# Optimization experiments

Hardware: AMD Instinct MI355X
Metric: run time of the kernel (lower is better)

The kernel has to match this reference:

```python
import jax, jax.numpy as jnp
import numpy as np

N = 20000   # num_nodes
D = 128     # node_dim
H = 128     # hidden_dim (also per-head channels, PyG out_channels is per-head)
EV = 64     # event_dim
NH = 4      # heads
E = 250000  # num edges
NT = 8      # num_event_types
K = 4       # active event types


def setup_inputs() -> dict:
    key = jax.random.key(0)
    ks = jax.random.split(key, 24)
    def w(i, shape, s=0.05):
        return jax.random.normal(ks[i], shape, dtype=jnp.float32) * s
    z = lambda shape: jnp.zeros(shape, jnp.float32)
    o = lambda shape: jnp.ones(shape, jnp.float32)
    return {
        "node_ids": jnp.arange(N, dtype=jnp.int32),
        "event_type_ids": jax.random.randint(ks[0], (K,), 0, NT, dtype=jnp.int32),
        "src": jax.random.randint(ks[1], (E,), 0, N, dtype=jnp.int32),
        "dst": jax.random.randint(ks[2], (E,), 0, N, dtype=jnp.int32),
        "event_features": jax.random.normal(ks[3], (EV,), dtype=jnp.float32),
        "event_intensity": jax.random.uniform(ks[4], (K,), dtype=jnp.float32),
        "node_emb_table": w(5, (N, D), 1.0),
        "event_type_table": w(6, (NT, H), 0.5),
        "ev_w1": w(7, (EV, H)), "ev_b1": z((H,)), "ev_g1": o((H,)), "ev_bt1": z((H,)),
        "ev_w2": w(8, (H, H)), "ev_b2": z((H,)), "ev_g2": o((H,)), "ev_bt2": z((H,)),
        "wq": w(9, (D + H, NH * H)), "bq": z((NH * H,)),
        "wk": w(10, (D + H, NH * H)), "bk": z((NH * H,)),
        "wv": w(11, (D + H, NH * H)), "bv": z((NH * H,)),
        "wskip": w(12, (D + H, H)), "bskip": z((H,)),
        "g0_w": w(13, (H, NH * H)), "g0_as": w(14, (NH, H), 0.1), "g0_ad": w(15, (NH, H), 0.1), "g0_b": z((H,)),
        "g1_w": w(16, (H, NH * H)), "g1_as": w(17, (NH, H), 0.1), "g1_ad": w(18, (NH, H), 0.1), "g1_b": z((H,)),
        "wih": w(19, (H, 4 * H)), "whh": w(20, (H, 4 * H)), "bih": z((4 * H,)), "bhh": z((4 * H,)),
    }


def layer_norm(x, g, b, eps=1e-5):
    mu = jnp.mean(x, axis=-1, keepdims=True)
    var = jnp.mean(jnp.square(x - mu), axis=-1, keepdims=True)
    return (x - mu) * jax.lax.rsqrt(var + eps) * g + b


def segment_softmax(logits, seg, n):
    # logits: [E, NH]; softmax over edges sharing the same destination seg id
    m = jax.ops.segment_max(logits, seg, num_segments=n)
    m = jnp.where(jnp.isfinite(m), m, 0.0)  # guard empty segments
    e = jnp.exp(logits - m[seg])
    s = jax.ops.segment_sum(e, seg, num_segments=n)
    return e / (s[seg] + 1e-16)


def _forward(node_ids, event_type_ids, src, dst,
             event_features, event_intensity, node_emb_table, event_type_table,
             ev_w1, ev_b1, ev_g1, ev_bt1, ev_w2, ev_b2, ev_g2, ev_bt2,
             wq, bq, wk, bk, wv, bv, wskip, bskip,
             g0_w, g0_as, g0_ad, g0_b, g1_w, g1_as, g1_ad, g1_b,
             wih, whh, bih, bhh):
    node_emb = node_emb_table[node_ids]                                      # [N, D]
    # event encoder MLP (dropout off / eval mode)
    e = jax.nn.relu(layer_norm(event_features @ ev_w1 + ev_b1, ev_g1, ev_bt1))
    e = jax.nn.relu(layer_norm(e @ ev_w2 + ev_b2, ev_g2, ev_bt2))            # [H]
    # intensity-weighted mean of active event-type embeddings
    e = e + jnp.mean(event_type_table[event_type_ids] * event_intensity[:, None], axis=0)
    x = jnp.concatenate([node_emb, jnp.broadcast_to(e, (N, H))], axis=1)     # [N, D+H]

    # --- TransformerConv (heads=NH, concat=False -> head mean, root_weight skip) ---
    q = (x @ wq + bq).reshape(N, NH, H)
    k = (x @ wk + bk).reshape(N, NH, H)
    v = (x @ wv + bv).reshape(N, NH, H)
    alpha = jnp.sum(q[dst] * k[src], axis=-1) / jnp.sqrt(jnp.float32(H))     # [E, NH]
    alpha = segment_softmax(alpha, dst, N)
    agg = jax.ops.segment_sum(v[src] * alpha[..., None], dst, num_segments=N)  # [N, NH, H]
    x = agg.mean(axis=1) + x @ wskip + bskip                                 # [N, H]

    sl = jnp.arange(N, dtype=src.dtype)
    src2 = jnp.concatenate([src, sl])
    dst2 = jnp.concatenate([dst, sl])
    for w_, asrc, adst, b_ in ((g0_w, g0_as, g0_ad, g0_b), (g1_w, g1_as, g1_ad, g1_b)):
        xh = (x @ w_).reshape(N, NH, H)
        a_s = jnp.sum(xh * asrc, axis=-1)                                    # [N, NH]
        a_d = jnp.sum(xh * adst, axis=-1)
        ee = jax.nn.leaky_relu(a_s[src2] + a_d[dst2], 0.2)                   # [E+N, NH]
        a = segment_softmax(ee, dst2, N)
        out = jax.ops.segment_sum(xh[src2] * a[..., None], dst2, num_segments=N)
        x = jax.nn.relu(out.mean(axis=1) + b_)                               # [N, H]

    # --- batched LSTMCell, zero initial (h, c); torch gate order i, f, g, o ---
    h0 = jnp.zeros((N, H), x.dtype)
    c0 = jnp.zeros((N, H), x.dtype)
    gates = x @ wih + bih + h0 @ whh + bhh                                   # [N, 4H]
    gi, gf, gg, go = jnp.split(gates, 4, axis=-1)
    c = jax.nn.sigmoid(gf) * c0 + jax.nn.sigmoid(gi) * jnp.tanh(gg)
    h = jax.nn.sigmoid(go) * jnp.tanh(c)
    return h, c


def reference(node_ids, event_type_ids, src, dst,
              event_features, event_intensity, node_emb_table, event_type_table,
              ev_w1, ev_b1, ev_g1, ev_bt1, ev_w2, ev_b2, ev_g2, ev_bt2,
              wq, bq, wk, bk, wv, bv, wskip, bskip,
              g0_w, g0_as, g0_ad, g0_b, g1_w, g1_as, g1_ad, g1_b,
              wih, whh, bih, bhh):
    return _forward(node_ids, event_type_ids, src, dst,
                    event_features, event_intensity, node_emb_table, event_type_table,
                    ev_w1, ev_b1, ev_g1, ev_bt1, ev_w2, ev_b2, ev_g2, ev_bt2,
                    wq, bq, wk, bk, wv, bv, wskip, bskip,
                    g0_w, g0_as, g0_ad, g0_b, g1_w, g1_as, g1_ad, g1_b,
                    wih, whh, bih, bhh)
```

## Files before the change

kernel.cpp:

```cpp
#include <hip/hip_runtime.h>
#include <math.h>

#define D_DIM 128
#define H_DIM 128
#define QKV_N 1664
#define SQRT_H_INV 0.08838834764831845f

typedef unsigned short u16;
typedef unsigned short ushort8v __attribute__((ext_vector_type(8)));
typedef __bf16 bf16x8 __attribute__((ext_vector_type(8)));
typedef float f32x4 __attribute__((ext_vector_type(4)));

__device__ __forceinline__ float grp16_sum(float v) {
  v += __shfl_xor(v, 1);
  v += __shfl_xor(v, 2);
  v += __shfl_xor(v, 4);
  v += __shfl_xor(v, 8);
  return v;
}

__device__ __forceinline__ void split_bf16(float x, u16& h, u16& l) {
  __bf16 hb = (__bf16)x;
  float rm = x - (float)hb;
  __bf16 lb = (__bf16)rm;
  h = __builtin_bit_cast(u16, hb);
  l = __builtin_bit_cast(u16, lb);
}

__global__ __launch_bounds__(128) void k_event(
    const float* __restrict__ ef, int EV,
    const float* __restrict__ w1, const float* __restrict__ b1,
    const float* __restrict__ g1, const float* __restrict__ bt1,
    const float* __restrict__ w2, const float* __restrict__ b2,
    const float* __restrict__ g2, const float* __restrict__ bt2,
    const float* __restrict__ ett, const int* __restrict__ etid,
    const float* __restrict__ inten, int K,
    float* __restrict__ e_out)
{
  __shared__ float sh[H_DIM];
  __shared__ float red[H_DIM];
  const int t = threadIdx.x;

  float acc = b1[t];
  for (int i = 0; i < EV; ++i) acc += ef[i] * w1[i * H_DIM + t];

  red[t] = acc; __syncthreads();
  for (int s = 64; s > 0; s >>= 1) { if (t < s) red[t] += red[t + s]; __syncthreads(); }
  float mu = red[0] / H_DIM; __syncthreads();
  float d = acc - mu;
  red[t] = d * d; __syncthreads();
  for (int s = 64; s > 0; s >>= 1) { if (t < s) red[t] += red[t + s]; __syncthreads(); }
  float var = red[0] / H_DIM; __syncthreads();
  float y = d * rsqrtf(var + 1e-5f) * g1[t] + bt1[t];
  y = fmaxf(y, 0.f);
  sh[t] = y; __syncthreads();

  float acc2 = b2[t];
  for (int i = 0; i < H_DIM; ++i) acc2 += sh[i] * w2[i * H_DIM + t];

  red[t] = acc2; __syncthreads();
  for (int s = 64; s > 0; s >>= 1) { if (t < s) red[t] += red[t + s]; __syncthreads(); }
  mu = red[0] / H_DIM; __syncthreads();
  d = acc2 - mu;
  red[t] = d * d; __syncthreads();
  for (int s = 64; s > 0; s >>= 1) { if (t < s) red[t] += red[t + s]; __syncthreads(); }
  var = red[0] / H_DIM; __syncthreads();
  float y2 = d * rsqrtf(var + 1e-5f) * g2[t] + bt2[t];
  y2 = fmaxf(y2, 0.f);

  float m = 0.f;
  for (int k = 0; k < K; ++k) m += ett[etid[k] * H_DIM + t] * inten[k];
  e_out[t] = y2 + m / (float)K;
}

__global__ __launch_bounds__(256) void k_cvec(
    const float* __restrict__ e,
    const float* __restrict__ wq, const float* __restrict__ bq,
    const float* __restrict__ wk, const float* __restrict__ bk,
    const float* __restrict__ wv, const float* __restrict__ bv,
    const float* __restrict__ wskip, const float* __restrict__ bskip,
    float* __restrict__ cvec)
{
  __shared__ float es[H_DIM];
  const int t = threadIdx.x;
  if (t < H_DIM) es[t] = e[t];
  __syncthreads();
  int j = blockIdx.x * 256 + t;
  if (j >= QKV_N) return;
  const float* W; const float* b; int col; int stride;
  if (j < 512)       { W = wq;    b = bq;    col = j;        stride = 512; }
  else if (j < 1024) { W = wk;    b = bk;    col = j - 512;  stride = 512; }
  else if (j < 1536) { W = wv;    b = bv;    col = j - 1024; stride = 512; }
  else               { W = wskip; b = bskip; col = j - 1536; stride = 128; }
  float a = b[col];
  for (int i = 0; i < H_DIM; ++i) a += es[i] * W[(D_DIM + i) * stride + col];
  cvec[j] = a;
}

__global__ __launch_bounds__(256) void k_pack(
    const float* __restrict__ wq, const float* __restrict__ wk,
    const float* __restrict__ wv, const float* __restrict__ wskip,
    float* __restrict__ B1)
{
  int idx = blockIdx.x * 256 + threadIdx.x;
  if (idx >= D_DIM * QKV_N) return;
  int i = idx / QKV_N, j = idx - i * QKV_N;
  float v;
  if (j < 512)       v = wq[i * 512 + j];
  else if (j < 1024) v = wk[i * 512 + (j - 512)];
  else if (j < 1536) v = wv[i * 512 + (j - 1024)];
  else               v = wskip[i * 128 + (j - 1536)];
  B1[idx] = v;
}

__global__ __launch_bounds__(256) void k_cvec2(
    const float* __restrict__ bih, const float* __restrict__ bhh,
    float* __restrict__ cvec2)
{
  int j = blockIdx.x * 256 + threadIdx.x;
  if (j < 512) cvec2[j] = bih[j] + bhh[j];
}

__global__ __launch_bounds__(256) void k_split_a(
    const float* __restrict__ A, const int* __restrict__ ids,
    u16* __restrict__ hi, u16* __restrict__ lo, int M, int Mpad)
{
  int idx = blockIdx.x * 256 + threadIdx.x;
  if (idx >= Mpad * 16) return;
  int row = idx >> 4, g = idx & 15;
  int gp = g ^ (row & 7);
  size_t dst = (size_t)row * 128 + gp * 8;
  if (row < M) {
    int ar = ids ? ids[row] : row;
    const float* srcp = A + (size_t)ar * 128 + g * 8;
#pragma unroll
    for (int j = 0; j < 8; ++j) {
      u16 h, l;
      split_bf16(srcp[j], h, l);
      hi[dst + j] = h; lo[dst + j] = l;
    }
  } else {
#pragma unroll
    for (int j = 0; j < 8; ++j) { hi[dst + j] = 0; lo[dst + j] = 0; }
  }
}

__global__ __launch_bounds__(256) void k_split_bt(
    const float* __restrict__ W,
    u16* __restrict__ hi, u16* __restrict__ lo, int Nc)
{
  int idx = blockIdx.x * 256 + threadIdx.x;
  if (idx >= Nc * 16) return;
  int n = idx >> 4, g = idx & 15;
  int gp = g ^ (n & 7);
  size_t dst = (size_t)n * 128 + gp * 8;
#pragma unroll
  for (int j = 0; j < 8; ++j) {
    u16 h, l;
    split_bf16(W[(size_t)(g * 8 + j) * Nc + n], h, l);
    hi[dst + j] = h; lo[dst + j] = l;
  }
}

__global__ __launch_bounds__(256, 2) void mfma_gemm(
    const u16* __restrict__ Ahi, const u16* __restrict__ Alo,
    const u16* __restrict__ Bhi, const u16* __restrict__ Blo,
    const float* __restrict__ cvec, float* __restrict__ C, int M, int Nn,
    u16* __restrict__ bf_out, int bf_lo, int bf_hi, int bf_stride, int skipf32)
{
  __shared__ u16 lds[32768];
  u16* As_hi = lds;
  u16* As_lo = lds + 8192;
  u16* Bs_hi = lds + 16384;
  u16* Bs_lo = lds + 24576;

  const int t = threadIdx.x;
  const int bm = blockIdx.y * 128;
  const int bn = blockIdx.x * 128;
  const int lane = t & 63;
  const int wid = t >> 6;
  const int wr = wid >> 1, wc = wid & 1;
  const int abase = wr * 64 + (lane & 15);
  const int bbase = wc * 64 + (lane & 15);

  int srow[4], sg[4];
#pragma unroll
  for (int i = 0; i < 4; ++i) {
    int idx = i * 256 + t;
    srow[i] = idx >> 3;
    sg[i] = idx & 7;
  }

  ushort8v ra_h[4], ra_l[4], rb_h[4], rb_l[4];

#pragma unroll
  for (int i = 0; i < 4; ++i) {
    size_t ga = (size_t)(bm + srow[i]) * 128 + sg[i] * 8;
    size_t gb = (size_t)(bn + srow[i]) * 128 + sg[i] * 8;
    ra_h[i] = *(const ushort8v*)&Ahi[ga];
    ra_l[i] = *(const ushort8v*)&Alo[ga];
    rb_h[i] = *(const ushort8v*)&Bhi[gb];
    rb_l[i] = *(const ushort8v*)&Blo[gb];
  }
#pragma unroll
  for (int i = 0; i < 4; ++i) {
    int lo_ = srow[i] * 64 + sg[i] * 8;
    *(ushort8v*)&As_hi[lo_] = ra_h[i];
    *(ushort8v*)&As_lo[lo_] = ra_l[i];
    *(ushort8v*)&Bs_hi[lo_] = rb_h[i];
    *(ushort8v*)&Bs_lo[lo_] = rb_l[i];
  }
  __syncthreads();

#pragma unroll
  for (int i = 0; i < 4; ++i) {
    size_t ga = (size_t)(bm + srow[i]) * 128 + 64 + sg[i] * 8;
    size_t gb = (size_t)(bn + srow[i]) * 128 + 64 + sg[i] * 8;
    ra_h[i] = *(const ushort8v*)&Ahi[ga];
    ra_l[i] = *(const ushort8v*)&Alo[ga];
    rb_h[i] = *(const ushort8v*)&Bhi[gb];
    rb_l[i] = *(const ushort8v*)&Blo[gb];
  }

  f32x4 acc[4][4];
  const f32x4 zero = {0.f, 0.f, 0.f, 0.f};
#pragma unroll
  for (int i = 0; i < 4; ++i)
#pragma unroll
    for (int j = 0; j < 4; ++j) acc[i][j] = zero;

#pragma unroll
  for (int ks = 0; ks < 2; ++ks) {
    const int gl = (((ks & 1) << 2) + (lane >> 4)) ^ (lane & 7);
    bf16x8 ah[4], al[4], bh[4], bl[4];
#pragma unroll
    for (int i = 0; i < 4; ++i) {
      int ra = (abase + i * 16) * 64 + gl * 8;
      ah[i] = *(const bf16x8*)&As_hi[ra];
      al[i] = *(const bf16x8*)&As_lo[ra];
      int rb = (bbase + i * 16) * 64 + gl * 8;
      bh[i] = *(const bf16x8*)&Bs_hi[rb];
      bl[i] = *(const bf16x8*)&Bs_lo[rb];
    }
#pragma unroll
    for (int i = 0; i < 4; ++i)
#pragma unroll
      for (int j = 0; j < 4; ++j) {
        acc[i][j] = __builtin_amdgcn_mfma_f32_16x16x32_bf16(ah[i], bh[j], acc[i][j], 0, 0, 0);
        acc[i][j] = __builtin_amdgcn_mfma_f32_16x16x32_bf16(ah[i], bl[j], acc[i][j], 0, 0, 0);
        acc[i][j] = __builtin_amdgcn_mfma_f32_16x16x32_bf16(al[i], bh[j], acc[i][j], 0, 0, 0);
      }
  }
  __syncthreads();

#pragma unroll
  for (int i = 0; i < 4; ++i) {
    int lo_ = srow[i] * 64 + sg[i] * 8;
    *(ushort8v*)&As_hi[lo_] = ra_h[i];
    *(ushort8v*)&As_lo[lo_] = ra_l[i];
    *(ushort8v*)&Bs_hi[lo_] = rb_h[i];
    *(ushort8v*)&Bs_lo[lo_] = rb_l[i];
  }
  __syncthreads();

#pragma unroll
  for (int ks = 2; ks < 4; ++ks) {
    const int gl = (((ks & 1) << 2) + (lane >> 4)) ^ (lane & 7);
    bf16x8 ah[4], al[4], bh[4], bl[4];
#pragma unroll
    for (int i = 0; i < 4; ++i) {
      int ra = (abase + i * 16) * 64 + gl * 8;
      ah[i] = *(const bf16x8*)&As_hi[ra];
      al[i] = *(const bf16x8*)&As_lo[ra];
      int rb = (bbase + i * 16) * 64 + gl * 8;
      bh[i] = *(const bf16x8*)&Bs_hi[rb];
      bl[i] = *(const bf16x8*)&Bs_lo[rb];
    }
#pragma unroll
    for (int i = 0; i < 4; ++i)
#pragma unroll
      for (int j = 0; j < 4; ++j) {
        acc[i][j] = __builtin_amdgcn_mfma_f32_16x16x32_bf16(ah[i], bh[j], acc[i][j], 0, 0, 0);
        acc[i][j] = __builtin_amdgcn_mfma_f32_16x16x32_bf16(ah[i], bl[j], acc[i][j], 0, 0, 0);
        acc[i][j] = __builtin_amdgcn_mfma_f32_16x16x32_bf16(al[i], bh[j], acc[i][j], 0, 0, 0);
      }
  }

  const int rq = (lane >> 4) << 2;
  const int cq = lane & 15;
#pragma unroll
  for (int j = 0; j < 4; ++j) {
    int col = bn + wc * 64 + j * 16 + cq;
    float cv = cvec ? cvec[col] : 0.f;
    bool inbf = bf_out && col >= bf_lo && col < bf_hi;
    bool wf32 = !(inbf && skipf32);
#pragma unroll
    for (int i = 0; i < 4; ++i) {
#pragma unroll
      for (int r = 0; r < 4; ++r) {
        int row = bm + wr * 64 + i * 16 + rq + r;
        if (row < M) {
          float val = acc[i][j][r] + cv;
          if (wf32) C[(size_t)row * Nn + col] = val;
          if (inbf) bf_out[(size_t)row * bf_stride + (col - bf_lo)] =
              __builtin_bit_cast(u16, (__bf16)val);
        }
      }
    }
  }
}

__global__ __launch_bounds__(256) void k_zero(int* __restrict__ p, int n) {
  int i = blockIdx.x * 256 + threadIdx.x;
  if (i < n) p[i] = 0;
}
__global__ __launch_bounds__(256) void k_count(
    const int* __restrict__ dst, int* __restrict__ counts, int E) {
  int e = blockIdx.x * 256 + threadIdx.x;
  if (e < E) atomicAdd(&counts[dst[e]], 1);
}
__global__ __launch_bounds__(1024) void k_scan(
    const int* __restrict__ counts, int* __restrict__ offs,
    int* __restrict__ cursor, int N)
{
  __shared__ int wsum[16];
  const int t = threadIdx.x;
  const int lane = t & 63;
  const int wid = t >> 6;
  int running = 0;
  for (int base = 0; base < N; base += 1024) {
    int v = (base + t < N) ? counts[base + t] : 0;
    int incl = v;
#pragma unroll
    for (int s = 1; s < 64; s <<= 1) {
      int u = __shfl_up(incl, s);
      if (lane >= s) incl += u;
    }
    if (lane == 63) wsum[wid] = incl;
    __syncthreads();
    if (wid == 0) {
      int w = (lane < 16) ? wsum[lane] : 0;
#pragma unroll
      for (int s = 1; s < 16; s <<= 1) {
        int u = __shfl_up(w, s);
        if (lane >= s) w += u;
      }
      if (lane < 16) wsum[lane] = w;
    }
    __syncthreads();
    int wpre = (wid > 0) ? wsum[wid - 1] : 0;
    int tot = wsum[15];
    int inclg = incl + wpre;
    if (base + t < N) {
      offs[base + t + 1] = running + inclg;
      cursor[base + t] = running + inclg - v;
    }
    running += tot;
    __syncthreads();
  }
  if (t == 0) offs[0] = 0;
}
__global__ __launch_bounds__(256) void k_fill(
    const int* __restrict__ src, const int* __restrict__ dst,
    int* __restrict__ cursor, int* __restrict__ csr_src, int E) {
  int e = blockIdx.x * 256 + threadIdx.x;
  if (e < E) {
    int slot = atomicAdd(&cursor[dst[e]], 1);
    csr_src[slot] = src[e];
  }
}

__global__ __launch_bounds__(256) void k_tconv(
    const float* __restrict__ C1, const u16* __restrict__ KV,
    const int* __restrict__ offs, const int* __restrict__ csr_src,
    u16* __restrict__ Xhi, u16* __restrict__ Xlo, int N)
{
  const int wid = threadIdx.x >> 6;
  const int lane = threadIdx.x & 63;
  const int node = blockIdx.x * 4 + wid;
  if (node >= N) {
    if (lane < 16) {
      size_t dst = (size_t)node * 128 + (size_t)((lane ^ (node & 7)) * 8);
#pragma unroll
      for (int j = 0; j < 8; ++j) { Xhi[dst + j] = 0; Xlo[dst + j] = 0; }
    }
    return;
  }
  const float* crow = C1 + (size_t)node * QKV_N;
  float q[8];
  {
    float4 q0 = *(const float4*)(crow + lane * 8);
    float4 q1 = *(const float4*)(crow + lane * 8 + 4);
    q[0]=q0.x; q[1]=q0.y; q[2]=q0.z; q[3]=q0.w;
    q[4]=q1.x; q[5]=q1.y; q[6]=q1.z; q[7]=q1.w;
  }
  const int beg = offs[node], end = offs[node + 1];
  float mx = -1e30f;
  float ssum = 0.f;
  float acc[8] = {0.f,0.f,0.f,0.f,0.f,0.f,0.f,0.f};

  int e = beg;
  for (; e + 4 <= end; e += 4) {
    int s0 = csr_src[e];
    int s1 = csr_src[e + 1];
    int s2 = csr_src[e + 2];
    int s3 = csr_src[e + 3];
    const u16* r0 = KV + (size_t)s0 * 1024 + lane * 8;
    const u16* r1 = KV + (size_t)s1 * 1024 + lane * 8;
    const u16* r2 = KV + (size_t)s2 * 1024 + lane * 8;
    const u16* r3 = KV + (size_t)s3 * 1024 + lane * 8;
    bf16x8 k0 = *(const bf16x8*)(r0);
    bf16x8 k1 = *(const bf16x8*)(r1);
    bf16x8 k2 = *(const bf16x8*)(r2);
    bf16x8 k3 = *(const bf16x8*)(r3);
    bf16x8 v0 = *(const bf16x8*)(r0 + 512);
    bf16x8 v1 = *(const bf16x8*)(r1 + 512);
    bf16x8 v2 = *(const bf16x8*)(r2 + 512);
    bf16x8 v3 = *(const bf16x8*)(r3 + 512);
    float p0 = 0.f, p1 = 0.f, p2 = 0.f, p3 = 0.f;
#pragma unroll
    for (int j = 0; j < 8; ++j) {
      p0 += q[j] * (float)k0[j];
      p1 += q[j] * (float)k1[j];
      p2 += q[j] * (float)k2[j];
      p3 += q[j] * (float)k3[j];
    }
    p0 = grp16_sum(p0) * SQRT_H_INV;
    p1 = grp16_sum(p1) * SQRT_H_INV;
    p2 = grp16_sum(p2) * SQRT_H_INV;
    p3 = grp16_sum(p3) * SQRT_H_INV;
    float nm = fmaxf(fmaxf(fmaxf(p0, p1), fmaxf(p2, p3)), mx);
    float sc = expf(mx - nm);
    float w0 = expf(p0 - nm);
    float w1 = expf(p1 - nm);
    float w2 = expf(p2 - nm);
    float w3 = expf(p3 - nm);
    ssum = ssum * sc + (w0 + w1) + (w2 + w3);
#pragma unroll
    for (int j = 0; j < 8; ++j)
      acc[j] = acc[j] * sc + (w0 * (float)v0[j] + w1 * (float)v1[j])
                           + (w2 * (float)v2[j] + w3 * (float)v3[j]);
    mx = nm;
  }
  for (; e < end; ++e) {
    int s0 = csr_src[e];
    const u16* r0 = KV + (size_t)s0 * 1024 + lane * 8;
    bf16x8 ka = *(const bf16x8*)(r0);
    bf16x8 va = *(const bf16x8*)(r0 + 512);
    float p0 = 0.f;
#pragma unroll
    for (int j = 0; j < 8; ++j) p0 += q[j] * (float)ka[j];
    p0 = grp16_sum(p0) * SQRT_H_INV;
    float nm = fmaxf(mx, p0);
    float sc = expf(mx - nm);
    float w0 = expf(p0 - nm);
    ssum = ssum * sc + w0;
#pragma unroll
    for (int j = 0; j < 8; ++j)
      acc[j] = acc[j] * sc + w0 * (float)va[j];
    mx = nm;
  }

  float inv = 1.f / (ssum + 1e-16f);
#pragma unroll
  for (int j = 0; j < 8; ++j) acc[j] *= inv;
#pragma unroll
  for (int j = 0; j < 8; ++j) {
    acc[j] += __shfl_xor(acc[j], 16);
    acc[j] += __shfl_xor(acc[j], 32);
  }
  if (lane < 16) {
    const float* sk = crow + 1536 + lane * 8;
    size_t dst = (size_t)node * 128 + (size_t)((lane ^ (node & 7)) * 8);
#pragma unroll
    for (int j = 0; j < 8; ++j) {
      float x = 0.25f * acc[j] + sk[j];
      u16 h, l;
      split_bf16(x, h, l);
      Xhi[dst + j] = h; Xlo[dst + j] = l;
    }
  }
}

__global__ __launch_bounds__(256) void k_gat_ad(
    const float* __restrict__ xh, const float* __restrict__ as_w,
    const float* __restrict__ ad_w, float* __restrict__ a_s,
    float* __restrict__ a_d, int N)
{
  const int wid = threadIdx.x >> 6;
  const int lane = threadIdx.x & 63;
  const int node = blockIdx.x * 4 + wid;
  if (node >= N) return;
  const int head = lane >> 4;
  const int c0 = (lane & 15) * 8;
  const float* xr = xh + (size_t)node * 512 + lane * 8;
  float4 x0 = *(const float4*)(xr);
  float4 x1_ = *(const float4*)(xr + 4);
  const float* aw = as_w + head * 128 + c0;
  const float* dw = ad_w + head * 128 + c0;
  float s1 = x0.x*aw[0] + x0.y*aw[1] + x0.z*aw[2] + x0.w*aw[3]
           + x1_.x*aw[4] + x1_.y*aw[5] + x1_.z*aw[6] + x1_.w*aw[7];
  float s2 = x0.x*dw[0] + x0.y*dw[1] + x0.z*dw[2] + x0.w*dw[3]
           + x1_.x*dw[4] + x1_.y*dw[5] + x1_.z*dw[6] + x1_.w*dw[7];
  s1 = grp16_sum(s1);
  s2 = grp16_sum(s2);
  if ((lane & 15) == 0) {
    a_s[node * 4 + head] = s1;
    a_d[node * 4 + head] = s2;
  }
}

__global__ __launch_bounds__(256) void k_gat_agg(
    const float* __restrict__ xh, const u16* __restrict__ xhb,
    const float* __restrict__ a_s, const float* __restrict__ a_d,
    const int* __restrict__ offs, const int* __restrict__ csr_src,
    const float* __restrict__ bias,
    u16* __restrict__ Xhi, u16* __restrict__ Xlo, int N)
{
  const int wid = threadIdx.x >> 6;
  const int lane = threadIdx.x & 63;
  const int node = blockIdx.x * 4 + wid;
  if (node >= N) {
    if (lane < 16) {
      size_t dst = (size_t)node * 128 + (size_t)((lane ^ (node & 7)) * 8);
#pragma unroll
      for (int j = 0; j < 8; ++j) { Xhi[dst + j] = 0; Xlo[dst + j] = 0; }
    }
    return;
  }
  const int head = lane >> 4;
  const float adn = a_d[node * 4 + head];
  const float asn = a_s[node * 4 + head];
  float lself = asn + adn;
  lself = lself >= 0.f ? lself : 0.2f * lself;

  float mx = lself;
  float ssum = 1.f;
  float acc[8];
  {
    const float* xr = xh + (size_t)node * 512 + lane * 8;
    float4 x0 = *(const float4*)(xr);
    float4 x1_ = *(const float4*)(xr + 4);
    acc[0]=x0.x; acc[1]=x0.y; acc[2]=x0.z; acc[3]=x0.w;
    acc[4]=x1_.x; acc[5]=x1_.y; acc[6]=x1_.z; acc[7]=x1_.w;
  }

  const int beg = offs[node], end = offs[node + 1];
  int e = beg;
  for (; e + 4 <= end; e += 4) {
    int s0 = csr_src[e];
    int s1 = csr_src[e + 1];
    int s2 = csr_src[e + 2];
    int s3 = csr_src[e + 3];
    float l0 = a_s[s0 * 4 + head];
    float l1 = a_s[s1 * 4 + head];
    float l2 = a_s[s2 * 4 + head];
    float l3 = a_s[s3 * 4 + head];
    const u16* r0 = xhb + (size_t)s0 * 512 + lane * 8;
    const u16* r1 = xhb + (size_t)s1 * 512 + lane * 8;
    const u16* r2 = xhb + (size_t)s2 * 512 + lane * 8;
    const u16* r3 = xhb + (size_t)s3 * 512 + lane * 8;
    bf16x8 xa = *(const bf16x8*)(r0);
    bf16x8 xb = *(const bf16x8*)(r1);
    bf16x8 xc = *(const bf16x8*)(r2);
    bf16x8 xd = *(const bf16x8*)(r3);
    l0 += adn; l1 += adn; l2 += adn; l3 += adn;
    l0 = l0 >= 0.f ? l0 : 0.2f * l0;
    l1 = l1 >= 0.f ? l1 : 0.2f * l1;
    l2 = l2 >= 0.f ? l2 : 0.2f * l2;
    l3 = l3 >= 0.f ? l3 : 0.2f * l3;
    float nm = fmaxf(fmaxf(fmaxf(l0, l1), fmaxf(l2, l3)), mx);
    float sc = expf(mx - nm);
    float w0 = expf(l0 - nm);
    float w1 = expf(l1 - nm);
    float w2 = expf(l2 - nm);
    float w3 = expf(l3 - nm);
    ssum = ssum * sc + (w0 + w1) + (w2 + w3);
#pragma unroll
    for (int j = 0; j < 8; ++j)
      acc[j] = acc[j] * sc + (w0 * (float)xa[j] + w1 * (float)xb[j])
                           + (w2 * (float)xc[j] + w3 * (float)xd[j]);
    mx = nm;
  }
  for (; e < end; ++e) {
    int s0 = csr_src[e];
    float l0 = a_s[s0 * 4 + head] + adn;
    l0 = l0 >= 0.f ? l0 : 0.2f * l0;
    const u16* r0 = xhb + (size_t)s0 * 512 + lane * 8;
    bf16x8 xa = *(const bf16x8*)(r0);
    float nm = fmaxf(mx, l0);
    float sc = expf(mx - nm);
    float w0 = expf(l0 - nm);
    ssum = ssum * sc + w0;
#pragma unroll
    for (int j = 0; j < 8; ++j)
      acc[j] = acc[j] * sc + w0 * (float)xa[j];
    mx = nm;
  }

  float inv = 1.f / (ssum + 1e-16f);
#pragma unroll
  for (int j = 0; j < 8; ++j) acc[j] *= inv;
#pragma unroll
  for (int j = 0; j < 8; ++j) {
    acc[j] += __shfl_xor(acc[j], 16);
    acc[j] += __shfl_xor(acc[j], 32);
  }
  if (lane < 16) {
    const float* b = bias + lane * 8;
    size_t dst = (size_t)node * 128 + (size_t)((lane ^ (node & 7)) * 8);
#pragma unroll
    for (int j = 0; j < 8; ++j) {
      float x = fmaxf(0.25f * acc[j] + b[j], 0.f);
      u16 h, l;
      split_bf16(x, h, l);
      Xhi[dst + j] = h; Xlo[dst + j] = l;
    }
  }
}

__global__ __launch_bounds__(256) void k_lstm(
    const float* __restrict__ gates, float* __restrict__ out, int N)
{
  int idx = blockIdx.x * 256 + threadIdx.x;
  if (idx >= N * 128) return;
  int n = idx >> 7, c = idx & 127;
  const float* g = gates + (size_t)n * 512;
  float gi = g[c], gg = g[256 + c], go = g[384 + c];
  float cv = (1.f / (1.f + expf(-gi))) * tanhf(gg);
  float hv = (1.f / (1.f + expf(-go))) * tanhf(cv);
  out[idx] = hv;
  out[(size_t)N * 128 + idx] = cv;
}

extern "C" void kernel_launch(void* const* d_in, const int* in_sizes, int n_in,
                              void* d_out, int out_size, void* d_ws, size_t ws_size,
                              hipStream_t stream) {
  const int*   node_ids = (const int*)d_in[0];
  const int*   etid     = (const int*)d_in[1];
  const int*   src      = (const int*)d_in[2];
  const int*   dst      = (const int*)d_in[3];
  const float* ef       = (const float*)d_in[4];
  const float* inten    = (const float*)d_in[5];
  const float* nemb     = (const float*)d_in[6];
  const float* ett      = (const float*)d_in[7];
  const float* ev_w1 = (const float*)d_in[8],  *ev_b1 = (const float*)d_in[9];
  const float* ev_g1 = (const float*)d_in[10], *ev_bt1 = (const float*)d_in[11];
  const float* ev_w2 = (const float*)d_in[12], *ev_b2 = (const float*)d_in[13];
  const float* ev_g2 = (const float*)d_in[14], *ev_bt2 = (const float*)d_in[15];
  const float* wq = (const float*)d_in[16], *bq = (const float*)d_in[17];
  const float* wk = (const float*)d_in[18], *bk = (const float*)d_in[19];
  const float* wv = (const float*)d_in[20], *bv = (const float*)d_in[21];
  const float* wskip = (const float*)d_in[22], *bskip = (const float*)d_in[23];
  const float* g0_w = (const float*)d_in[24], *g0_as = (const float*)d_in[25];
  const float* g0_ad = (const float*)d_in[26], *g0_b = (const float*)d_in[27];
  const float* g1_w = (const float*)d_in[28], *g1_as = (const float*)d_in[29];
  const float* g1_ad = (const float*)d_in[30], *g1_b = (const float*)d_in[31];
  const float* wih = (const float*)d_in[32];
  const float* bih = (const float*)d_in[34], *bhh = (const float*)d_in[35];

  const int N = in_sizes[0];
  const int K = in_sizes[1];
  const int E = in_sizes[2];
  const int EV = in_sizes[4];

  const int gridMy = (N + 127) / 128;
  const int Npad = gridMy * 128;

  float* ws = (float*)d_ws;
  size_t o = 0;
  float* e_vec = ws + o; o += 128;
  float* cvec1 = ws + o; o += QKV_N;
  float* cvec2 = ws + o; o += 512;
  float* B1    = ws + o; o += (size_t)128 * QKV_N;
  float* C1    = ws + o; o += (size_t)N * QKV_N;
  float* xh    = ws + o; o += (size_t)N * 512;
  u16* Ahi  = (u16*)(ws + o); o += (size_t)Npad * 64;
  u16* Alo  = (u16*)(ws + o); o += (size_t)Npad * 64;
  u16* XShi = (u16*)(ws + o); o += (size_t)Npad * 64;
  u16* XSlo = (u16*)(ws + o); o += (size_t)Npad * 64;
  u16* Bqhi = (u16*)(ws + o); o += (size_t)QKV_N * 64;
  u16* Bqlo = (u16*)(ws + o); o += (size_t)QKV_N * 64;
  u16* Bg0hi = (u16*)(ws + o); o += 512 * 64;
  u16* Bg0lo = (u16*)(ws + o); o += 512 * 64;
  u16* Bg1hi = (u16*)(ws + o); o += 512 * 64;
  u16* Bg1lo = (u16*)(ws + o); o += 512 * 64;
  u16* Bwhi  = (u16*)(ws + o); o += 512 * 64;
  u16* Bwlo  = (u16*)(ws + o); o += 512 * 64;
  u16* KV   = (u16*)(ws + o); o += (size_t)Npad * 512;
  u16* xhb  = (u16*)(ws + o); o += (size_t)Npad * 256;
  float* a_s   = ws + o; o += (size_t)N * 4;
  float* a_d   = ws + o; o += (size_t)N * 4;
  int* counts  = (int*)(ws + o); o += N;
  int* offs    = (int*)(ws + o); o += (size_t)N + 1;
  int* cursor  = (int*)(ws + o); o += N;
  int* csr_src = (int*)(ws + o); o += E;

  float* out = (float*)d_out;

  const int nodeBlocks = (N + 3) / 4;
  const int nodeBlocksPad = Npad / 4;

  k_event<<<1, 128, 0, stream>>>(ef, EV, ev_w1, ev_b1, ev_g1, ev_bt1,
                                 ev_w2, ev_b2, ev_g2, ev_bt2,
                                 ett, etid, inten, K, e_vec);
  k_cvec<<<(QKV_N + 255) / 256, 256, 0, stream>>>(e_vec, wq, bq, wk, bk, wv, bv,
                                                  wskip, bskip, cvec1);
  k_pack<<<(D_DIM * QKV_N + 255) / 256, 256, 0, stream>>>(wq, wk, wv, wskip, B1);
  k_cvec2<<<2, 256, 0, stream>>>(bih, bhh, cvec2);

  k_split_a<<<(Npad * 16 + 255) / 256, 256, 0, stream>>>(nemb, node_ids, Ahi, Alo, N, Npad);
  k_split_bt<<<(QKV_N * 16 + 255) / 256, 256, 0, stream>>>(B1, Bqhi, Bqlo, QKV_N);
  k_split_bt<<<(512 * 16 + 255) / 256, 256, 0, stream>>>(g0_w, Bg0hi, Bg0lo, 512);
  k_split_bt<<<(512 * 16 + 255) / 256, 256, 0, stream>>>(g1_w, Bg1hi, Bg1lo, 512);
  k_split_bt<<<(512 * 16 + 255) / 256, 256, 0, stream>>>(wih, Bwhi, Bwlo, 512);

  k_zero<<<(N + 255) / 256, 256, 0, stream>>>(counts, N);
  k_count<<<(E + 255) / 256, 256, 0, stream>>>(dst, counts, E);
  k_scan<<<1, 1024, 0, stream>>>(counts, offs, cursor, N);
  k_fill<<<(E + 255) / 256, 256, 0, stream>>>(src, dst, cursor, csr_src, E);

  mfma_gemm<<<dim3(QKV_N / 128, gridMy), 256, 0, stream>>>(
      Ahi, Alo, Bqhi, Bqlo, cvec1, C1, N, QKV_N,
      KV, 512, 1536, 1024, 1);

  k_tconv<<<nodeBlocksPad, 256, 0, stream>>>(C1, KV, offs, csr_src, XShi, XSlo, N);

  mfma_gemm<<<dim3(4, gridMy), 256, 0, stream>>>(
      XShi, XSlo, Bg0hi, Bg0lo, nullptr, xh, N, 512,
      xhb, 0, 512, 512, 0);
  k_gat_ad<<<nodeBlocks, 256, 0, stream>>>(xh, g0_as, g0_ad, a_s, a_d, N);
  k_gat_agg<<<nodeBlocksPad, 256, 0, stream>>>(xh, xhb, a_s, a_d, offs, csr_src,
                                               g0_b, XShi, XSlo, N);

  mfma_gemm<<<dim3(4, gridMy), 256, 0, stream>>>(
      XShi, XSlo, Bg1hi, Bg1lo, nullptr, xh, N, 512,
      xhb, 0, 512, 512, 0);
  k_gat_ad<<<nodeBlocks, 256, 0, stream>>>(xh, g1_as, g1_ad, a_s, a_d, N);
  k_gat_agg<<<nodeBlocksPad, 256, 0, stream>>>(xh, xhb, a_s, a_d, offs, csr_src,
                                               g1_b, XShi, XSlo, N);

  mfma_gemm<<<dim3(4, gridMy), 256, 0, stream>>>(
      XShi, XSlo, Bwhi, Bwlo, cvec2, xh, N, 512,
      nullptr, 0, 0, 0, 0);
  k_lstm<<<((N * 128) + 255) / 256, 256, 0, stream>>>(xh, out, N);
}
```

Measured before the change: 445.8 us.

## Fuse GAT attention scores into GEMM epilogue, drop f32 outputs and dead LSTM gate

Merges the weight packing, splitting and bias kernels into one k_split_all and one k_cvec_all launch. The QKV GEMM now writes Q/K/V only as bf16 plus a small f32 skip buffer, instead of a full f32 C1 matrix. The GAT GEMMs compute the per-head source and destination attention dot products in the epilogue using LDS atomics, which removes k_gat_ad and the f32 xh writes; gat_agg reads its self term from bf16. The LSTM GEMM skips the forget-gate columns, which are unused because the initial cell state is zero. Together these cut launches and global memory traffic, at the cost of bf16 rounding on Q and the self-feature terms and extra LDS atomics in the epilogue.

```diff
diff --git a/kernel.cpp b/kernel.cpp
--- a/kernel.cpp
+++ b/kernel.cpp
@@ -3,8 +3,12 @@
 
 #define D_DIM 128
 #define H_DIM 128
-#define QKV_N 1664
 #define SQRT_H_INV 0.08838834764831845f
+#define BCOL_QKV 0
+#define BCOL_G0 1664
+#define BCOL_G1 2176
+#define BCOL_W  2688
+#define BCOL_TOT 3072
 
 typedef unsigned short u16;
 typedef unsigned short ushort8v __attribute__((ext_vector_type(8)));
@@ -73,52 +77,62 @@
   e_out[t] = y2 + m / (float)K;
 }
 
-__global__ __launch_bounds__(256) void k_cvec(
+__global__ __launch_bounds__(256) void k_cvec_all(
     const float* __restrict__ e,
     const float* __restrict__ wq, const float* __restrict__ bq,
     const float* __restrict__ wk, const float* __restrict__ bk,
     const float* __restrict__ wv, const float* __restrict__ bv,
     const float* __restrict__ wskip, const float* __restrict__ bskip,
-    float* __restrict__ cvec)
+    const float* __restrict__ bih, const float* __restrict__ bhh,
+    float* __restrict__ cvec1, float* __restrict__ cvec2)
 {
   __shared__ float es[H_DIM];
   const int t = threadIdx.x;
   if (t < H_DIM) es[t] = e[t];
   __syncthreads();
   int j = blockIdx.x * 256 + t;
-  if (j >= QKV_N) return;
-  const float* W; const float* b; int col; int stride;
-  if (j < 512)       { W = wq;    b = bq;    col = j;        stride = 512; }
-  else if (j < 1024) { W = wk;    b = bk;    col = j - 512;  stride = 512; }
-  else if (j < 1536) { W = wv;    b = bv;    col = j - 1024; stride = 512; }
-  else               { W = wskip; b = bskip; col = j - 1536; stride = 128; }
-  float a = b[col];
-  for (int i = 0; i < H_DIM; ++i) a += es[i] * W[(D_DIM + i) * stride + col];
-  cvec[j] = a;
-}
-
-__global__ __launch_bounds__(256) void k_pack(
+  if (j < 1664) {
+    const float* W; const float* b; int col; int stride;
+    if (j < 512)       { W = wq;    b = bq;    col = j;        stride = 512; }
+    else if (j < 1024) { W = wk;    b = bk;    col = j - 512;  stride = 512; }
+    else if (j < 1536) { W = wv;    b = bv;    col = j - 1024; stride = 512; }
+    else               { W = wskip; b = bskip; col = j - 1536; stride = 128; }
+    float a = b[col];
+    for (int i = 0; i < H_DIM; ++i) a += es[i] * W[(D_DIM + i) * stride + col];
+    cvec1[j] = a;
+  } else if (j < 1664 + 384) {
+    int j2 = j - 1664;
+    int src = (j2 < 128) ? j2 : j2 + 128;
+    cvec2[j2] = bih[src] + bhh[src];
+  }
+}
+
+__global__ __launch_bounds__(256) void k_split_all(
     const float* __restrict__ wq, const float* __restrict__ wk,
     const float* __restrict__ wv, const float* __restrict__ wskip,
-    float* __restrict__ B1)
+    const float* __restrict__ g0w, const float* __restrict__ g1w,
+    const float* __restrict__ wih,
+    u16* __restrict__ hi, u16* __restrict__ lo)
 {
   int idx = blockIdx.x * 256 + threadIdx.x;
-  if (idx >= D_DIM * QKV_N) return;
-  int i = idx / QKV_N, j = idx - i * QKV_N;
-  float v;
-  if (j < 512)       v = wq[i * 512 + j];
-  else if (j < 1024) v = wk[i * 512 + (j - 512)];
-  else if (j < 1536) v = wv[i * 512 + (j - 1024)];
-  else               v = wskip[i * 128 + (j - 1536)];
-  B1[idx] = v;
-}
-
-__global__ __launch_bounds__(256) void k_cvec2(
-    const float* __restrict__ bih, const float* __restrict__ bhh,
-    float* __restrict__ cvec2)
-{
-  int j = blockIdx.x * 256 + threadIdx.x;
-  if (j < 512) cvec2[j] = bih[j] + bhh[j];
+  if (idx >= BCOL_TOT * 16) return;
+  int n = idx >> 4, g = idx & 15;
+  const float* W; int col, stride;
+  if (n < 512)        { W = wq;    col = n;        stride = 512; }
+  else if (n < 1024)  { W = wk;    col = n - 512;  stride = 512; }
+  else if (n < 1536)  { W = wv;    col = n - 1024; stride = 512; }
+  else if (n < 1664)  { W = wskip; col = n - 1536; stride = 128; }
+  else if (n < 2176)  { W = g0w;   col = n - 1664; stride = 512; }
+  else if (n < 2688)  { W = g1w;   col = n - 2176; stride = 512; }
+  else { int c = n - 2688; W = wih; col = (c < 128) ? c : c + 128; stride = 512; }
+  int gp = g ^ (n & 7);
+  size_t dst = (size_t)n * 128 + gp * 8;
+#pragma unroll
+  for (int j = 0; j < 8; ++j) {
+    u16 h, l;
+    split_bf16(W[(size_t)(g * 8 + j) * stride + col], h, l);
+    hi[dst + j] = h; lo[dst + j] = l;
+  }
 }
 
 __global__ __launch_bounds__(256) void k_split_a(
@@ -145,28 +159,15 @@
   }
 }
 
-__global__ __launch_bounds__(256) void k_split_bt(
-    const float* __restrict__ W,
-    u16* __restrict__ hi, u16* __restrict__ lo, int Nc)
-{
-  int idx = blockIdx.x * 256 + threadIdx.x;
-  if (idx >= Nc * 16) return;
-  int n = idx >> 4, g = idx & 15;
-  int gp = g ^ (n & 7);
-  size_t dst = (size_t)n * 128 + gp * 8;
-#pragma unroll
-  for (int j = 0; j < 8; ++j) {
-    u16 h, l;
-    split_bf16(W[(size_t)(g * 8 + j) * Nc + n], h, l);
-    hi[dst + j] = h; lo[dst + j] = l;
-  }
-}
-
 __global__ __launch_bounds__(256, 2) void mfma_gemm(
     const u16* __restrict__ Ahi, const u16* __restrict__ Alo,
     const u16* __restrict__ Bhi, const u16* __restrict__ Blo,
-    const float* __restrict__ cvec, float* __restrict__ C, int M, int Nn,
-    u16* __restrict__ bf_out, int bf_lo, int bf_hi, int bf_stride, int skipf32)
+    const float* __restrict__ cvec,
+    u16* __restrict__ bf_out, int bf_cols,
+    float* __restrict__ f32_out, int f32_lo, int ld_f32,
+    const float* __restrict__ asw, const float* __restrict__ adw,
+    float* __restrict__ a_s, float* __restrict__ a_d,
+    int M)
 {
   __shared__ u16 lds[32768];
   u16* As_hi = lds;
@@ -288,23 +289,59 @@
 
   const int rq = (lane >> 4) << 2;
   const int cq = lane & 15;
-#pragma unroll
-  for (int j = 0; j < 4; ++j) {
-    int col = bn + wc * 64 + j * 16 + cq;
-    float cv = cvec ? cvec[col] : 0.f;
-    bool inbf = bf_out && col >= bf_lo && col < bf_hi;
-    bool wf32 = !(inbf && skipf32);
-#pragma unroll
-    for (int i = 0; i < 4; ++i) {
-#pragma unroll
-      for (int r = 0; r < 4; ++r) {
-        int row = bm + wr * 64 + i * 16 + rq + r;
-        if (row < M) {
-          float val = acc[i][j][r] + cv;
-          if (wf32) C[(size_t)row * Nn + col] = val;
-          if (inbf) bf_out[(size_t)row * bf_stride + (col - bf_lo)] =
-              __builtin_bit_cast(u16, (__bf16)val);
+  const int head = bn >> 7;
+
+  float ws_[4], wd_[4];
+  float* redS = (float*)lds;
+  float* redD = ((float*)lds) + 128;
+  if (asw) {
+#pragma unroll
+    for (int j = 0; j < 4; ++j) {
+      int cc = (wc * 64 + j * 16 + cq) & 127;
+      ws_[j] = asw[head * 128 + cc];
+      wd_[j] = adw[head * 128 + cc];
+    }
+    __syncthreads();
+    if (t < 128) { redS[t] = 0.f; }
+    else if (t < 256) { redD[t - 128] = 0.f; }
+    __syncthreads();
+  }
+
+#pragma unroll
+  for (int i = 0; i < 4; ++i) {
+#pragma unroll
+    for (int r = 0; r < 4; ++r) {
+      int rowl = wr * 64 + i * 16 + rq + r;
+      int row = bm + rowl;
+      bool rok = row < M;
+      float ps = 0.f, pd = 0.f;
+#pragma unroll
+      for (int j = 0; j < 4; ++j) {
+        int col = bn + wc * 64 + j * 16 + cq;
+        float a = acc[i][j][r];
+        if (rok) {
+          float val = a + (cvec ? cvec[col] : 0.f);
+          if (bf_out && col < bf_cols)
+            bf_out[(size_t)row * bf_cols + col] =
+                __builtin_bit_cast(u16, (__bf16)val);
+          if (f32_out && col >= f32_lo)
+            f32_out[(size_t)row * ld_f32 + (col - f32_lo)] = val;
         }
+        if (asw) { ps += a * ws_[j]; pd += a * wd_[j]; }
+      }
+      if (asw && rok) {
+        atomicAdd(&redS[rowl], ps);
+        atomicAdd(&redD[rowl], pd);
+      }
+    }
+  }
+  if (asw) {
+    __syncthreads();
+    if (t < 128) {
+      int row = bm + t;
+      if (row < M) {
+        a_s[row * 4 + head] = redS[t];
+        a_d[row * 4 + head] = redD[t];
       }
     }
   }
@@ -371,7 +408,7 @@
 }
 
 __global__ __launch_bounds__(256) void k_tconv(
-    const float* __restrict__ C1, const u16* __restrict__ KV,
+    const u16* __restrict__ QKVp, const float* __restrict__ skipbuf,
     const int* __restrict__ offs, const int* __restrict__ csr_src,
     u16* __restrict__ Xhi, u16* __restrict__ Xlo, int N)
 {
@@ -386,13 +423,11 @@
     }
     return;
   }
-  const float* crow = C1 + (size_t)node * QKV_N;
   float q[8];
   {
-    float4 q0 = *(const float4*)(crow + lane * 8);
-    float4 q1 = *(const float4*)(crow + lane * 8 + 4);
-    q[0]=q0.x; q[1]=q0.y; q[2]=q0.z; q[3]=q0.w;
-    q[4]=q1.x; q[5]=q1.y; q[6]=q1.z; q[7]=q1.w;
+    bf16x8 qv = *(const bf16x8*)(QKVp + (size_t)node * 1536 + lane * 8);
+#pragma unroll
+    for (int j = 0; j < 8; ++j) q[j] = (float)qv[j];
   }
   const int beg = offs[node], end = offs[node + 1];
   float mx = -1e30f;
@@ -405,10 +440,10 @@
     int s1 = csr_src[e + 1];
     int s2 = csr_src[e + 2];
     int s3 = csr_src[e + 3];
-    const u16* r0 = KV + (size_t)s0 * 1024 + lane * 8;
-    const u16* r1 = KV + (size_t)s1 * 1024 + lane * 8;
-    const u16* r2 = KV + (size_t)s2 * 1024 + lane * 8;
-    const u16* r3 = KV + (size_t)s3 * 1024 + lane * 8;
+    const u16* r0 = QKVp + (size_t)s0 * 1536 + 512 + lane * 8;
+    const u16* r1 = QKVp + (size_t)s1 * 1536 + 512 + lane * 8;
+    const u16* r2 = QKVp + (size_t)s2 * 1536 + 512 + lane * 8;
+    const u16* r3 = QKVp + (size_t)s3 * 1536 + 512 + lane * 8;
     bf16x8 k0 = *(const bf16x8*)(r0);
     bf16x8 k1 = *(const bf16x8*)(r1);
     bf16x8 k2 = *(const bf16x8*)(r2);
@@ -444,7 +479,7 @@
   }
   for (; e < end; ++e) {
     int s0 = csr_src[e];
-    const u16* r0 = KV + (size_t)s0 * 1024 + lane * 8;
+    const u16* r0 = QKVp + (size_t)s0 * 1536 + 512 + lane * 8;
     bf16x8 ka = *(const bf16x8*)(r0);
     bf16x8 va = *(const bf16x8*)(r0 + 512);
     float p0 = 0.f;
@@ -470,7 +505,7 @@
     acc[j] += __shfl_xor(acc[j], 32);
   }
   if (lane < 16) {
-    const float* sk = crow + 1536 + lane * 8;
+    const float* sk = skipbuf + (size_t)node * 128 + lane * 8;
     size_t dst = (size_t)node * 128 + (size_t)((lane ^ (node & 7)) * 8);
 #pragma unroll
     for (int j = 0; j < 8; ++j) {
@@ -482,36 +517,8 @@
   }
 }
 
-__global__ __launch_bounds__(256) void k_gat_ad(
-    const float* __restrict__ xh, const float* __restrict__ as_w,
-    const float* __restrict__ ad_w, float* __restrict__ a_s,
-    float* __restrict__ a_d, int N)
-{
-  const int wid = threadIdx.x >> 6;
-  const int lane = threadIdx.x & 63;
-  const int node = blockIdx.x * 4 + wid;
-  if (node >= N) return;
-  const int head = lane >> 4;
-  const int c0 = (lane & 15) * 8;
-  const float* xr = xh + (size_t)node * 512 + lane * 8;
-  float4 x0 = *(const float4*)(xr);
-  float4 x1_ = *(const float4*)(xr + 4);
-  const float* aw = as_w + head * 128 + c0;
-  const float* dw = ad_w + head * 128 + c0;
-  float s1 = x0.x*aw[0] + x0.y*aw[1] + x0.z*aw[2] + x0.w*aw[3]
-           + x1_.x*aw[4] + x1_.y*aw[5] + x1_.z*aw[6] + x1_.w*aw[7];
-  float s2 = x0.x*dw[0] + x0.y*dw[1] + x0.z*dw[2] + x0.w*dw[3]
-           + x1_.x*dw[4] + x1_.y*dw[5] + x1_.z*dw[6] + x1_.w*dw[7];
-  s1 = grp16_sum(s1);
-  s2 = grp16_sum(s2);
-  if ((lane & 15) == 0) {
-    a_s[node * 4 + head] = s1;
-    a_d[node * 4 + head] = s2;
-  }
-}
-
 __global__ __launch_bounds__(256) void k_gat_agg(
-    const float* __restrict__ xh, const u16* __restrict__ xhb,
+    const u16* __restrict__ xhb,
     const float* __restrict__ a_s, const float* __restrict__ a_d,
     const int* __restrict__ offs, const int* __restrict__ csr_src,
     const float* __restrict__ bias,
@@ -538,11 +545,9 @@
   float ssum = 1.f;
   float acc[8];
   {
-    const float* xr = xh + (size_t)node * 512 + lane * 8;
-    float4 x0 = *(const float4*)(xr);
-    float4 x1_ = *(const float4*)(xr + 4);
-    acc[0]=x0.x; acc[1]=x0.y; acc[2]=x0.z; acc[3]=x0.w;
-    acc[4]=x1_.x; acc[5]=x1_.y; acc[6]=x1_.z; acc[7]=x1_.w;
+    bf16x8 xs = *(const bf16x8*)(xhb + (size_t)node * 512 + lane * 8);
+#pragma unroll
+    for (int j = 0; j < 8; ++j) acc[j] = (float)xs[j];
   }
 
   const int beg = offs[node], end = offs[node + 1];
@@ -625,8 +630,8 @@
   int idx = blockIdx.x * 256 + threadIdx.x;
   if (idx >= N * 128) return;
   int n = idx >> 7, c = idx & 127;
-  const float* g = gates + (size_t)n * 512;
-  float gi = g[c], gg = g[256 + c], go = g[384 + c];
+  const float* g = gates + (size_t)n * 384;
+  float gi = g[c], gg = g[128 + c], go = g[256 + c];
   float cv = (1.f / (1.f + expf(-gi))) * tanhf(gg);
   float hv = (1.f / (1.f + expf(-go))) * tanhf(cv);
   out[idx] = hv;
@@ -670,25 +675,18 @@
   float* ws = (float*)d_ws;
   size_t o = 0;
   float* e_vec = ws + o; o += 128;
-  float* cvec1 = ws + o; o += QKV_N;
-  float* cvec2 = ws + o; o += 512;
-  float* B1    = ws + o; o += (size_t)128 * QKV_N;
-  float* C1    = ws + o; o += (size_t)N * QKV_N;
-  float* xh    = ws + o; o += (size_t)N * 512;
+  float* cvec1 = ws + o; o += 1664;
+  float* cvec2 = ws + o; o += 384;
+  u16* Ballhi = (u16*)(ws + o); o += (size_t)BCOL_TOT * 64;
+  u16* Balllo = (u16*)(ws + o); o += (size_t)BCOL_TOT * 64;
   u16* Ahi  = (u16*)(ws + o); o += (size_t)Npad * 64;
   u16* Alo  = (u16*)(ws + o); o += (size_t)Npad * 64;
   u16* XShi = (u16*)(ws + o); o += (size_t)Npad * 64;
   u16* XSlo = (u16*)(ws + o); o += (size_t)Npad * 64;
-  u16* Bqhi = (u16*)(ws + o); o += (size_t)QKV_N * 64;
-  u16* Bqlo = (u16*)(ws + o); o += (size_t)QKV_N * 64;
-  u16* Bg0hi = (u16*)(ws + o); o += 512 * 64;
-  u16* Bg0lo = (u16*)(ws + o); o += 512 * 64;
-  u16* Bg1hi = (u16*)(ws + o); o += 512 * 64;
-  u16* Bg1lo = (u16*)(ws + o); o += 512 * 64;
-  u16* Bwhi  = (u16*)(ws + o); o += 512 * 64;
-  u16* Bwlo  = (u16*)(ws + o); o += 512 * 64;
-  u16* KV   = (u16*)(ws + o); o += (size_t)Npad * 512;
+  u16* QKVp = (u16*)(ws + o); o += (size_t)Npad * 768;
+  float* skipbuf = ws + o; o += (size_t)Npad * 128;
   u16* xhb  = (u16*)(ws + o); o += (size_t)Npad * 256;
+  float* gates = ws + o; o += (size_t)Npad * 384;
   float* a_s   = ws + o; o += (size_t)N * 4;
   float* a_d   = ws + o; o += (size_t)N * 4;
   int* counts  = (int*)(ws + o); o += N;
@@ -697,51 +695,47 @@
   int* csr_src = (int*)(ws + o); o += E;
 
   float* out = (float*)d_out;
-
-  const int nodeBlocks = (N + 3) / 4;
   const int nodeBlocksPad = Npad / 4;
 
   k_event<<<1, 128, 0, stream>>>(ef, EV, ev_w1, ev_b1, ev_g1, ev_bt1,
                                  ev_w2, ev_b2, ev_g2, ev_bt2,
                                  ett, etid, inten, K, e_vec);
-  k_cvec<<<(QKV_N + 255) / 256, 256, 0, stream>>>(e_vec, wq, bq, wk, bk, wv, bv,
-                                                  wskip, bskip, cvec1);
-  k_pack<<<(D_DIM * QKV_N + 255) / 256, 256, 0, stream>>>(wq, wk, wv, wskip, B1);
-  k_cvec2<<<2, 256, 0, stream>>>(bih, bhh, cvec2);
-
+  k_cvec_all<<<8, 256, 0, stream>>>(e_vec, wq, bq, wk, bk, wv, bv,
+                                    wskip, bskip, bih, bhh, cvec1, cvec2);
+  k_split_all<<<(BCOL_TOT * 16) / 256, 256, 0, stream>>>(
+      wq, wk, wv, wskip, g0_w, g1_w, wih, Ballhi, Balllo);
   k_split_a<<<(Npad * 16 + 255) / 256, 256, 0, stream>>>(nemb, node_ids, Ahi, Alo, N, Npad);
-  k_split_bt<<<(QKV_N * 16 + 255) / 256, 256, 0, stream>>>(B1, Bqhi, Bqlo, QKV_N);
-  k_split_bt<<<(512 * 16 + 255) / 256, 256, 0, stream>>>(g0_w, Bg0hi, Bg0lo, 512);
-  k_split_bt<<<(512 * 16 + 255) / 256, 256, 0, stream>>>(g1_w, Bg1hi, Bg1lo, 512);
-  k_split_bt<<<(512 * 16 + 255) / 256, 256, 0, stream>>>(wih, Bwhi, Bwlo, 512);
 
   k_zero<<<(N + 255) / 256, 256, 0, stream>>>(counts, N);
   k_count<<<(E + 255) / 256, 256, 0, stream>>>(dst, counts, E);
   k_scan<<<1, 1024, 0, stream>>>(counts, offs, cursor, N);
   k_fill<<<(E + 255) / 256, 256, 0, stream>>>(src, dst, cursor, csr_src, E);
 
-  mfma_gemm<<<dim3(QKV_N / 128, gridMy), 256, 0, stream>>>(
-      Ahi, Alo, Bqhi, Bqlo, cvec1, C1, N, QKV_N,
-      KV, 512, 1536, 1024, 1);
-
-  k_tconv<<<nodeBlocksPad, 256, 0, stream>>>(C1, KV, offs, csr_src, XShi, XSlo, N);
+  mfma_gemm<<<dim3(13, gridMy), 256, 0, stream>>>(
+      Ahi, Alo, Ballhi + (size_t)BCOL_QKV * 128, Balllo + (size_t)BCOL_QKV * 128,
+      cvec1, QKVp, 1536, skipbuf, 1536, 128,
+      nullptr, nullptr, nullptr, nullptr, N);
+
+  k_tconv<<<nodeBlocksPad, 256, 0, stream>>>(QKVp, skipbuf, offs, csr_src,
+                                             XShi, XSlo, N);
 
   mfma_gemm<<<dim3(4, gridMy), 256, 0, stream>>>(
-      XShi, XSlo, Bg0hi, Bg0lo, nullptr, xh, N, 512,
-      xhb, 0, 512, 512, 0);
-  k_gat_ad<<<nodeBlocks, 256, 0, stream>>>(xh, g0_as, g0_ad, a_s, a_d, N);
-  k_gat_agg<<<nodeBlocksPad, 256, 0, stream>>>(xh, xhb, a_s, a_d, offs, csr_src,
+      XShi, XSlo, Ballhi + (size_t)BCOL_G0 * 128, Balllo + (size_t)BCOL_G0 * 128,
+      nullptr, xhb, 512, nullptr, 0, 0,
+      g0_as, g0_ad, a_s, a_d, N);
+  k_gat_agg<<<nodeBlocksPad, 256, 0, stream>>>(xhb, a_s, a_d, offs, csr_src,
                                                g0_b, XShi, XSlo, N);
 
   mfma_gemm<<<dim3(4, gridMy), 256, 0, stream>>>(
-      XShi, XSlo, Bg1hi, Bg1lo, nullptr, xh, N, 512,
-      xhb, 0, 512, 512, 0);
-  k_gat_ad<<<nodeBlocks, 256, 0, stream>>>(xh, g1_as, g1_ad, a_s, a_d, N);
-  k_gat_agg<<<nodeBlocksPad, 256, 0, stream>>>(xh, xhb, a_s, a_d, offs, csr_src,
+      XShi, XSlo, Ballhi + (size_t)BCOL_G1 * 128, Balllo + (size_t)BCOL_G1 * 128,
+      nullptr, xhb, 512, nullptr, 0, 0,
+      g1_as, g1_ad, a_s, a_d, N);
+  k_gat_agg<<<nodeBlocksPad, 256, 0, stream>>>(xhb, a_s, a_d, offs, csr_src,
                                                g1_b, XShi, XSlo, N);
 
-  mfma_gemm<<<dim3(4, gridMy), 256, 0, stream>>>(
-      XShi, XSlo, Bwhi, Bwlo, cvec2, xh, N, 512,
-      nullptr, 0, 0, 0, 0);
-  k_lstm<<<((N * 128) + 255) / 256, 256, 0, stream>>>(xh, out, N);
-}
+  mfma_gemm<<<dim3(3, gridMy), 256, 0, stream>>>(
+      XShi, XSlo, Ballhi + (size_t)BCOL_W * 128, Balllo + (size_t)BCOL_W * 128,
+      cvec2, nullptr, 0, gates, 0, 384,
+      nullptr, nullptr, nullptr, nullptr, N);
+  k_lstm<<<((N * 128) + 255) / 256, 256, 0, stream>>>(gates, out, N);
+}
```

Result: no change. 453.3 us (+1.7%).
